# Optimization experiments

Measured on AMD Instinct MI355X. Metric: run time of the kernel, lower is better.

## Reference

```python
import jax, jax.numpy as jnp
import numpy as np
from jax import lax

B, C_IN, H, W = 32, 128, 64, 64
E = 384           # embed_dim
EB = E // 3       # per-branch channels
RED = 16          # ChannelAttention reduction -> hidden 384//16 = 24


def _conv(x, w, b, k):
    # x: [B,C,H,W], w: [O,I,k,k] (OIHW), 'same' padding k//2, stride 1
    p = k // 2
    y = lax.conv_general_dilated(x, w, (1, 1), [(p, p), (p, p)],
                                 dimension_numbers=('NCHW', 'OIHW', 'NCHW'))
    return y + b[None, :, None, None]


def setup_inputs() -> dict:
    key = jax.random.key(0)
    ks = jax.random.split(key, 8)

    def he(k, shape, fan_k, cout):
        fan_out = fan_k * fan_k * cout
        return jax.random.normal(k, shape, jnp.float32) * np.sqrt(2.0 / fan_out)

    x = jax.random.normal(ks[0], (B, C_IN, H, W), jnp.float32)
    w3 = he(ks[1], (EB, C_IN, 3, 3), 3, EB)
    w5 = he(ks[2], (EB, C_IN, 5, 5), 5, EB)
    w7 = he(ks[3], (EB, C_IN, 7, 7), 7, EB)
    ca_w1 = jax.random.normal(ks[4], (E // RED, E), jnp.float32) * 0.02
    ca_w2 = jax.random.normal(ks[5], (E, E // RED), jnp.float32) * 0.02
    fusion_w = he(ks[6], (E, E), 1, E)
    return {
        'x': x,
        'w3': w3, 'b3': jnp.zeros((EB,), jnp.float32),
        'w5': w5, 'b5': jnp.zeros((EB,), jnp.float32),
        'w7': w7, 'b7': jnp.zeros((EB,), jnp.float32),
        'ca_w1': ca_w1, 'ca_w2': ca_w2,
        'fusion_w': fusion_w, 'fusion_b': jnp.zeros((E,), jnp.float32),
        'ln_g': jnp.ones((E,), jnp.float32), 'ln_b': jnp.zeros((E,), jnp.float32),
    }


def reference(x, w3, b3, w5, b5, w7, b7, ca_w1, ca_w2, fusion_w, fusion_b, ln_g, ln_b):
    # multi-scale conv branches (strides all 1 -> identical HxW, no interpolation needed)
    f3 = _conv(x, w3, b3, 3)
    f5 = _conv(x, w5, b5, 5)
    f7 = _conv(x, w7, b7, 7)
    fused = jnp.concatenate([f3, f5, f7], axis=1)        # [B, E, H, W]

    # ChannelAttention (CBAM-style): shared MLP over global avg & max pool, sigmoid gate
    avg = jnp.mean(fused, axis=(2, 3))                   # [B, E]
    mx = jnp.max(fused, axis=(2, 3))                     # [B, E]
    def mlp(v):
        return jax.nn.relu(v @ ca_w1.T) @ ca_w2.T
    attn = jax.nn.sigmoid(mlp(avg) + mlp(mx))            # [B, E]
    fused = fused * attn[:, :, None, None]

    # 1x1 fusion conv
    fused = jnp.einsum('bchw,oc->bohw', fused, fusion_w) + fusion_b[None, :, None, None]

    # flatten to tokens + LayerNorm
    Bb, Ee, Hh, Ww = fused.shape
    t = fused.reshape(Bb, Ee, Hh * Ww).transpose(0, 2, 1)  # [B, N, E]
    mu = jnp.mean(t, axis=-1, keepdims=True)
    var = jnp.var(t, axis=-1, keepdims=True)
    t = (t - mu) / jnp.sqrt(var + 1e-5) * ln_g + ln_b
    return t
```

## Files before the change

### kernel.cpp

```cpp
#include <hip/hip_runtime.h>

#define BB 32
#define CIN 128
#define HH 64
#define WW 64
#define EE 384
#define EBC 128
#define HID 24
#define NPIX (HH*WW)
#define NTOK (BB*NPIX)

typedef __attribute__((ext_vector_type(8))) short short8;
typedef __attribute__((ext_vector_type(4))) float f32x4;
typedef __attribute__((ext_vector_type(4))) unsigned short us4;

__device__ __forceinline__ unsigned short f2bf(float f) {
    unsigned u = __float_as_uint(f);
    unsigned r = u + 0x7fffu + ((u >> 16) & 1u);
    return (unsigned short)(r >> 16);
}
__device__ __forceinline__ float bf2f(unsigned short u) {
    return __uint_as_float(((unsigned)u) << 16);
}
__device__ __forceinline__ unsigned fmapu(float f) {
    unsigned u = __float_as_uint(f);
    return (u & 0x80000000u) ? ~u : (u | 0x80000000u);
}
__device__ __forceinline__ float funmap(unsigned u) {
    unsigned b = (u & 0x80000000u) ? (u ^ 0x80000000u) : ~u;
    return __uint_as_float(b);
}

__global__ void repack_x(const float* __restrict__ x, unsigned short* __restrict__ xh) {
    int y = blockIdx.x, b = blockIdx.y;
    __shared__ unsigned short t[CIN][WW + 6];
    const float* xp = x + (((size_t)b * CIN) * HH + y) * WW;
    #pragma unroll
    for (int it = 0; it < 32; ++it) {
        int xc = threadIdx.x & 63;
        int c = (threadIdx.x >> 6) + it * 4;
        t[c][xc] = f2bf(xp[(size_t)c * NPIX + xc]);
    }
    __syncthreads();
    unsigned short* op = xh + (((size_t)b * HH + y) * WW) * CIN;
    #pragma unroll
    for (int it = 0; it < 8; ++it) {
        int id = threadIdx.x + it * 256;
        int xc = id >> 5, c0 = (id & 31) * 4;
        us4 v = { t[c0][xc], t[c0 + 1][xc], t[c0 + 2][xc], t[c0 + 3][xc] };
        *(us4*)(op + xc * CIN + c0) = v;
    }
}

__global__ void repack_w(const float* __restrict__ w3, const float* __restrict__ w5,
                         const float* __restrict__ w7, const float* __restrict__ fw,
                         unsigned short* __restrict__ wrep, unsigned short* __restrict__ fwb,
                         float* __restrict__ psum, unsigned* __restrict__ pmax) {
    int idx = blockIdx.x * 256 + threadIdx.x;
    if (idx < 83 * 16384) {
        int j = idx & 7;
        int lane = (idx >> 3) & 63;
        int mt = (idx >> 9) & 7;
        int cb = (idx >> 12) & 3;
        int t = idx >> 14;
        int l16 = lane & 15, g4 = lane >> 4;
        int o = mt * 16 + l16;
        int c = cb * 32 + g4 * 8 + j;
        float v;
        if (t < 9)       { int tt = t;      int dy = tt / 3, dx = tt % 3; v = w3[((o * CIN + c) * 3 + dy) * 3 + dx]; }
        else if (t < 34) { int tt = t - 9;  int dy = tt / 5, dx = tt % 5; v = w5[((o * CIN + c) * 5 + dy) * 5 + dx]; }
        else             { int tt = t - 34; int dy = tt / 7, dx = tt % 7; v = w7[((o * CIN + c) * 7 + dy) * 7 + dx]; }
        wrep[idx] = f2bf(v);
    }
    if (idx < EE * EE) {
        int j = idx & 7;
        int lane = (idx >> 3) & 63;
        int mc = idx >> 9;
        int m = mc % 24, cb = mc / 24;
        int l16 = lane & 15, g4 = lane >> 4;
        int o = m * 16 + l16;
        int c = cb * 32 + g4 * 8 + j;
        fwb[idx] = f2bf(fw[o * EE + c]);
    }
    if (idx < BB * EE) { psum[idx] = 0.f; pmax[idx] = 0u; }
}

template <int KS>
__global__ __launch_bounds__(256, (KS == 7 ? 3 : 4)) void conv_mfma(
        const unsigned short* __restrict__ xh, const unsigned short* __restrict__ wrp,
        const float* __restrict__ bias, unsigned short* __restrict__ fused,
        float* __restrict__ psum, unsigned* __restrict__ pmax, int choff) {
    constexpr int PK = KS / 2;
    constexpr int RT = 4 + 2 * PK;
    constexpr int TPX = 64 + 2 * PK;
    constexpr int NCH = RT * 4 * TPX;

    __shared__ short8 smem[NCH];

    int b = blockIdx.z;
    int half = blockIdx.y;
    int y0 = blockIdx.x * 4;
    int lane = threadIdx.x & 63, wv = threadIdx.x >> 6;
    int l16 = lane & 15, g4 = lane >> 4;

    f32x4 acc[4][4];
    #pragma unroll
    for (int i = 0; i < 4; ++i)
        #pragma unroll
        for (int j = 0; j < 4; ++j) acc[i][j] = (f32x4){0.f, 0.f, 0.f, 0.f};

    const unsigned short* xb = xh + (size_t)b * (HH * WW * CIN);
    const short8* wv8 = (const short8*)wrp;

    for (int cb = 0; cb < 4; ++cb) {
        if (cb) __syncthreads();
        for (int i = threadIdx.x; i < NCH; i += 256) {
            int g = i & 3;
            int rp = i >> 2;
            int p = rp % TPX;
            int r = rp / TPX;
            int iy = y0 + r - PK, ix = p - PK;
            short8 v = {};
            if ((unsigned)iy < (unsigned)HH && (unsigned)ix < (unsigned)WW)
                v = *(const short8*)(xb + ((iy * WW + ix) * CIN + cb * 32 + g * 8));
            smem[(r * 4 + g) * TPX + p] = v;
        }
        __syncthreads();

        #pragma unroll 1
        for (int dy = 0; dy < KS; ++dy) {
            int lrow = ((wv + dy) * 4 + g4) * TPX + l16;
            #pragma unroll
            for (int dx = 0; dx < KS; ++dx) {
                const short8* wf = wv8 + (((size_t)(((dy * KS + dx) * 4 + cb) * 8) + half * 4) * 64 + lane);
                short8 a[4];
                #pragma unroll
                for (int mt = 0; mt < 4; ++mt)
                    a[mt] = wf[mt * 64];
                #pragma unroll
                for (int nt = 0; nt < 4; ++nt) {
                    short8 bf = smem[lrow + dx + nt * 16];
                    #pragma unroll
                    for (int mt = 0; mt < 4; ++mt)
                        acc[mt][nt] = __builtin_amdgcn_mfma_f32_16x16x32_bf16(a[mt], bf, acc[mt][nt], 0, 0, 0);
                }
            }
        }
    }

    int y = y0 + wv;
    #pragma unroll
    for (int mt = 0; mt < 4; ++mt) {
        int orow = half * 64 + mt * 16 + g4 * 4;
        f32x4 bv = *(const f32x4*)(bias + orow);
        float sacc[4] = {0.f, 0.f, 0.f, 0.f};
        float macc[4] = {-1e30f, -1e30f, -1e30f, -1e30f};
        #pragma unroll
        for (int nt = 0; nt < 4; ++nt) {
            int pix = y * WW + nt * 16 + l16;
            us4 pk;
            #pragma unroll
            for (int r = 0; r < 4; ++r) {
                float vv = acc[mt][nt][r] + bv[r];
                sacc[r] += vv;
                macc[r] = fmaxf(macc[r], vv);
                pk[r] = f2bf(vv);
            }
            *(us4*)(fused + ((size_t)(b * NPIX + pix)) * EE + choff + orow) = pk;
        }
        #pragma unroll
        for (int r = 0; r < 4; ++r) {
            float s = sacc[r], m = macc[r];
            #pragma unroll
            for (int sh = 1; sh < 16; sh <<= 1) {
                s += __shfl_xor(s, sh);
                m = fmaxf(m, __shfl_xor(m, sh));
            }
            if (l16 == 0) {
                atomicAdd(&psum[b * EE + choff + orow + r], s);
                atomicMax(&pmax[b * EE + choff + orow + r], fmapu(m));
            }
        }
    }
}

__global__ void attn_kernel(const float* __restrict__ psum, const unsigned* __restrict__ pmax,
                            const float* __restrict__ ca_w1, const float* __restrict__ ca_w2,
                            float* __restrict__ attn) {
    int b = blockIdx.x;
    __shared__ float av[EE], mxv[EE], hsum[HID];
    int t = threadIdx.x;
    if (t < EE) {
        av[t] = psum[b * EE + t] * (1.0f / (float)NPIX);
        mxv[t] = funmap(pmax[b * EE + t]);
    }
    __syncthreads();
    if (t < HID) {
        float sa = 0.f, sm = 0.f;
        for (int c = 0; c < EE; ++c) {
            float w = ca_w1[t * EE + c];
            sa += w * av[c];
            sm += w * mxv[c];
        }
        hsum[t] = fmaxf(sa, 0.f) + fmaxf(sm, 0.f);
    }
    __syncthreads();
    if (t < EE) {
        float s = 0.f;
        for (int h = 0; h < HID; ++h) s += ca_w2[t * HID + h] * hsum[h];
        attn[b * EE + t] = 1.f / (1.f + __expf(-s));
    }
}

#define BPITCH 392
__global__ __launch_bounds__(256, 2) void fuse_ln(
        const unsigned short* __restrict__ fused, const unsigned short* __restrict__ fwb,
        const float* __restrict__ attn,
        const float* __restrict__ fusion_b, const float* __restrict__ ln_g,
        const float* __restrict__ ln_b, float* __restrict__ out) {
    int b = blockIdx.y;
    int p0 = blockIdx.x * 64;
    int lane = threadIdx.x & 63, wv = threadIdx.x >> 6;
    int l16 = lane & 15, g4 = lane >> 4;

    __shared__ unsigned short sB[64 * BPITCH];
    __shared__ float sattn[EE];
    __shared__ float s_sum[4][64], s_sq[4][64], s_mean[64], s_rstd[64];

    for (int i = threadIdx.x; i < EE; i += 256) sattn[i] = attn[b * EE + i];
    __syncthreads();

    const unsigned short* fb = fused + ((size_t)(b * NPIX + p0)) * EE;
    for (int i = threadIdx.x; i < 64 * 48; i += 256) {
        int cg = i % 48, tok = i / 48;
        short8 raw = *(const short8*)(fb + tok * EE + cg * 8);
        short8 o;
        #pragma unroll
        for (int j = 0; j < 8; ++j)
            o[j] = (short)f2bf(bf2f((unsigned short)raw[j]) * sattn[cg * 8 + j]);
        *(short8*)(sB + tok * BPITCH + cg * 8) = o;
    }
    __syncthreads();

    f32x4 acc[6][4];
    #pragma unroll
    for (int i = 0; i < 6; ++i)
        #pragma unroll
        for (int j = 0; j < 4; ++j) acc[i][j] = (f32x4){0.f, 0.f, 0.f, 0.f};

    const short8* fw8 = (const short8*)fwb;
    for (int cb = 0; cb < 12; ++cb) {
        int c0 = cb * 32 + g4 * 8;
        short8 a[6];
        #pragma unroll
        for (int mt = 0; mt < 6; ++mt)
            a[mt] = fw8[(cb * 24 + wv * 6 + mt) * 64 + lane];
        #pragma unroll
        for (int nt = 0; nt < 4; ++nt) {
            short8 bf = *(const short8*)(sB + (nt * 16 + l16) * BPITCH + c0);
            #pragma unroll
            for (int mt = 0; mt < 6; ++mt)
                acc[mt][nt] = __builtin_amdgcn_mfma_f32_16x16x32_bf16(a[mt], bf, acc[mt][nt], 0, 0, 0);
        }
    }

    #pragma unroll
    for (int nt = 0; nt < 4; ++nt) {
        float ps = 0.f, pq = 0.f;
        #pragma unroll
        for (int mt = 0; mt < 6; ++mt) {
            int o = wv * 96 + mt * 16 + g4 * 4;
            f32x4 bv = *(const f32x4*)(fusion_b + o);
            #pragma unroll
            for (int r = 0; r < 4; ++r) {
                float v = acc[mt][nt][r] + bv[r];
                acc[mt][nt][r] = v;
                ps += v;
                pq += v * v;
            }
        }
        ps += __shfl_xor(ps, 16); pq += __shfl_xor(pq, 16);
        ps += __shfl_xor(ps, 32); pq += __shfl_xor(pq, 32);
        if (g4 == 0) { s_sum[wv][nt * 16 + l16] = ps; s_sq[wv][nt * 16 + l16] = pq; }
    }
    __syncthreads();
    if (threadIdx.x < 64) {
        int pix = threadIdx.x;
        float s = 0.f, q = 0.f;
        #pragma unroll
        for (int w = 0; w < 4; ++w) { s += s_sum[w][pix]; q += s_sq[w][pix]; }
        float mean = s * (1.0f / (float)EE);
        float var = q * (1.0f / (float)EE) - mean * mean;
        s_mean[pix] = mean;
        s_rstd[pix] = rsqrtf(var + 1e-5f);
    }
    __syncthreads();

    #pragma unroll
    for (int nt = 0; nt < 4; ++nt) {
        int pix = nt * 16 + l16;
        float mean = s_mean[pix], rstd = s_rstd[pix];
        size_t tokbase = ((size_t)(b * NPIX + p0 + pix)) * EE;
        #pragma unroll
        for (int mt = 0; mt < 6; ++mt) {
            int o = wv * 96 + mt * 16 + g4 * 4;
            f32x4 g = *(const f32x4*)(ln_g + o);
            f32x4 be = *(const f32x4*)(ln_b + o);
            f32x4 res;
            #pragma unroll
            for (int r = 0; r < 4; ++r)
                res[r] = (acc[mt][nt][r] - mean) * rstd * g[r] + be[r];
            *(f32x4*)(out + tokbase + o) = res;
        }
    }
}

extern "C" void kernel_launch(void* const* d_in, const int* in_sizes, int n_in,
                              void* d_out, int out_size, void* d_ws, size_t ws_size,
                              hipStream_t stream) {
    const float* x    = (const float*)d_in[0];
    const float* w3   = (const float*)d_in[1];
    const float* b3   = (const float*)d_in[2];
    const float* w5   = (const float*)d_in[3];
    const float* b5   = (const float*)d_in[4];
    const float* w7   = (const float*)d_in[5];
    const float* b7   = (const float*)d_in[6];
    const float* caw1 = (const float*)d_in[7];
    const float* caw2 = (const float*)d_in[8];
    const float* fw   = (const float*)d_in[9];
    const float* fbias= (const float*)d_in[10];
    const float* lng  = (const float*)d_in[11];
    const float* lnb  = (const float*)d_in[12];
    float* out = (float*)d_out;

    char* ws = (char*)d_ws;
    size_t off = 0;
    unsigned short* xh   = (unsigned short*)(ws + off); off += (size_t)BB * HH * WW * CIN * 2;
    unsigned short* wrep = (unsigned short*)(ws + off); off += (size_t)83 * EBC * CIN * 2;
    unsigned short* fwb  = (unsigned short*)(ws + off); off += (size_t)EE * EE * 2;
    unsigned short* fused= (unsigned short*)(ws + off); off += (size_t)NTOK * EE * 2;
    float*    psum = (float*)(ws + off);    off += (size_t)BB * EE * 4;
    unsigned* pmax = (unsigned*)(ws + off); off += (size_t)BB * EE * 4;
    float*    attn = (float*)(ws + off);    off += (size_t)BB * EE * 4;

    repack_x<<<dim3(HH, BB), 256, 0, stream>>>(x, xh);
    repack_w<<<dim3(5312), 256, 0, stream>>>(w3, w5, w7, fw, wrep, fwb, psum, pmax);

    conv_mfma<3><<<dim3(16, 2, BB), 256, 0, stream>>>(xh, wrep + 0 * 16384,  b3, fused, psum, pmax, 0);
    conv_mfma<5><<<dim3(16, 2, BB), 256, 0, stream>>>(xh, wrep + 9 * 16384,  b5, fused, psum, pmax, 128);
    conv_mfma<7><<<dim3(16, 2, BB), 256, 0, stream>>>(xh, wrep + 34 * 16384, b7, fused, psum, pmax, 256);

    attn_kernel<<<dim3(BB), 384, 0, stream>>>(psum, pmax, caw1, caw2, attn);
    fuse_ln<<<dim3(NPIX / 64, BB), 256, 0, stream>>>(fused, fwb, attn, fbias, lng, lnb, out);
}
```

Measured before the change: 708.1 us.

## Compute all 128 output channels per conv block with double-buffered weight loads

Each conv block now computes all 128 output channels (8 M-tiles) instead of splitting them across two blocks by grid y, so each input tile in LDS is staged once and reused across twice as many MFMAs. The tap loop is fully unrolled, and weight fragments for the next tap are prefetched into a second register set while the current tap's MFMAs run. This doubles the accumulator and weight register footprint, so launch bounds drop to 2 blocks per CU. The grid also halves to 512 blocks per branch, which lowers occupancy and parallelism.

Result: no change. 712.7 us (+0.7%).

```diff
diff --git a/kernel.cpp b/kernel.cpp
--- a/kernel.cpp
+++ b/kernel.cpp
@@ -86,7 +86,7 @@
 }
 
 template <int KS>
-__global__ __launch_bounds__(256, (KS == 7 ? 3 : 4)) void conv_mfma(
+__global__ __launch_bounds__(256, 2) void conv_mfma(
         const unsigned short* __restrict__ xh, const unsigned short* __restrict__ wrp,
         const float* __restrict__ bias, unsigned short* __restrict__ fused,
         float* __restrict__ psum, unsigned* __restrict__ pmax, int choff) {
@@ -94,18 +94,18 @@
     constexpr int RT = 4 + 2 * PK;
     constexpr int TPX = 64 + 2 * PK;
     constexpr int NCH = RT * 4 * TPX;
+    constexpr int NT = KS * KS;
 
     __shared__ short8 smem[NCH];
 
     int b = blockIdx.z;
-    int half = blockIdx.y;
     int y0 = blockIdx.x * 4;
     int lane = threadIdx.x & 63, wv = threadIdx.x >> 6;
     int l16 = lane & 15, g4 = lane >> 4;
 
-    f32x4 acc[4][4];
-    #pragma unroll
-    for (int i = 0; i < 4; ++i)
+    f32x4 acc[8][4];
+    #pragma unroll
+    for (int i = 0; i < 8; ++i)
         #pragma unroll
         for (int j = 0; j < 4; ++j) acc[i][j] = (f32x4){0.f, 0.f, 0.f, 0.f};
 
@@ -127,31 +127,38 @@
         }
         __syncthreads();
 
-        #pragma unroll 1
-        for (int dy = 0; dy < KS; ++dy) {
-            int lrow = ((wv + dy) * 4 + g4) * TPX + l16;
-            #pragma unroll
-            for (int dx = 0; dx < KS; ++dx) {
-                const short8* wf = wv8 + (((size_t)(((dy * KS + dx) * 4 + cb) * 8) + half * 4) * 64 + lane);
-                short8 a[4];
+        short8 a0[8], a1[8];
+        {
+            const short8* wf = wv8 + ((size_t)(cb * 8)) * 64 + lane;
+            #pragma unroll
+            for (int mt = 0; mt < 8; ++mt) a0[mt] = wf[mt * 64];
+        }
+        #pragma unroll
+        for (int t = 0; t < NT; ++t) {
+            short8* ac = (t & 1) ? a1 : a0;
+            short8* an = (t & 1) ? a0 : a1;
+            if (t + 1 < NT) {
+                const short8* wf = wv8 + ((size_t)(((t + 1) * 4 + cb) * 8)) * 64 + lane;
                 #pragma unroll
-                for (int mt = 0; mt < 4; ++mt)
-                    a[mt] = wf[mt * 64];
+                for (int mt = 0; mt < 8; ++mt) an[mt] = wf[mt * 64];
+            }
+            int dy = t / KS, dx = t % KS;
+            int lrow = ((wv + dy) * 4 + g4) * TPX + l16 + dx;
+            short8 bfv[4];
+            #pragma unroll
+            for (int nt = 0; nt < 4; ++nt) bfv[nt] = smem[lrow + nt * 16];
+            #pragma unroll
+            for (int nt = 0; nt < 4; ++nt)
                 #pragma unroll
-                for (int nt = 0; nt < 4; ++nt) {
-                    short8 bf = smem[lrow + dx + nt * 16];
-                    #pragma unroll
-                    for (int mt = 0; mt < 4; ++mt)
-                        acc[mt][nt] = __builtin_amdgcn_mfma_f32_16x16x32_bf16(a[mt], bf, acc[mt][nt], 0, 0, 0);
-                }
-            }
+                for (int mt = 0; mt < 8; ++mt)
+                    acc[mt][nt] = __builtin_amdgcn_mfma_f32_16x16x32_bf16(ac[mt], bfv[nt], acc[mt][nt], 0, 0, 0);
         }
     }
 
     int y = y0 + wv;
     #pragma unroll
-    for (int mt = 0; mt < 4; ++mt) {
-        int orow = half * 64 + mt * 16 + g4 * 4;
+    for (int mt = 0; mt < 8; ++mt) {
+        int orow = mt * 16 + g4 * 4;
         f32x4 bv = *(const f32x4*)(bias + orow);
         float sacc[4] = {0.f, 0.f, 0.f, 0.f};
         float macc[4] = {-1e30f, -1e30f, -1e30f, -1e30f};
@@ -346,9 +353,9 @@
     repack_x<<<dim3(HH, BB), 256, 0, stream>>>(x, xh);
     repack_w<<<dim3(5312), 256, 0, stream>>>(w3, w5, w7, fw, wrep, fwb, psum, pmax);
 
-    conv_mfma<3><<<dim3(16, 2, BB), 256, 0, stream>>>(xh, wrep + 0 * 16384,  b3, fused, psum, pmax, 0);
-    conv_mfma<5><<<dim3(16, 2, BB), 256, 0, stream>>>(xh, wrep + 9 * 16384,  b5, fused, psum, pmax, 128);
-    conv_mfma<7><<<dim3(16, 2, BB), 256, 0, stream>>>(xh, wrep + 34 * 16384, b7, fused, psum, pmax, 256);
+    conv_mfma<3><<<dim3(16, 1, BB), 256, 0, stream>>>(xh, wrep + 0 * 16384,  b3, fused, psum, pmax, 0);
+    conv_mfma<5><<<dim3(16, 1, BB), 256, 0, stream>>>(xh, wrep + 9 * 16384,  b5, fused, psum, pmax, 128);
+    conv_mfma<7><<<dim3(16, 1, BB), 256, 0, stream>>>(xh, wrep + 34 * 16384, b7, fused, psum, pmax, 256);
 
     attn_kernel<<<dim3(BB), 384, 0, stream>>>(psum, pmax, caw1, caw2, attn);
     fuse_ln<<<dim3(NPIX / 64, BB), 256, 0, stream>>>(fused, fwb, attn, fbias, lng, lnb, out);
```
